# Optimization experiments

Measured on AMD Instinct MI355X. Metric: run time of the kernel, lower is better.

Reference implementation:

```python
import jax, jax.numpy as jnp
import numpy as np

NC = 80
CENTER_RADIUS = 2.5
TOPK = 10
BOX_W, CLS_W, OBJ_W = 7.5, 0.5, 1.0
ALPHA, GAMMA = 0.25, 2.0
EPS = 1e-7
BIG = 1e10


def _corners(b):
    x, y, w, h = b[..., 0], b[..., 1], b[..., 2], b[..., 3]
    return x - w / 2, y - h / 2, x + w / 2, y + h / 2


def _pairwise_iou(b1, b2):
    # b1: (N,4) xywh, b2: (G,4) xywh -> (N,G) plain IoU
    x11, y11, x12, y12 = [t[:, None] for t in _corners(b1)]
    x21, y21, x22, y22 = _corners(b2)
    inter = jnp.clip(jnp.minimum(x12, x22) - jnp.maximum(x11, x21), 0) * \
            jnp.clip(jnp.minimum(y12, y22) - jnp.maximum(y11, y21), 0)
    union = (b1[:, 2] * b1[:, 3])[:, None] + (b2[:, 2] * b2[:, 3])[None, :] - inter + EPS
    return inter / union


def _ciou(b1, b2):
    # aligned boxes (N,4),(N,4) xywh -> (N,) CIoU
    x11, y11, x12, y12 = _corners(b1)
    x21, y21, x22, y22 = _corners(b2)
    w1, h1 = b1[..., 2], b1[..., 3]
    w2, h2 = b2[..., 2], b2[..., 3]
    inter = jnp.clip(jnp.minimum(x12, x22) - jnp.maximum(x11, x21), 0) * \
            jnp.clip(jnp.minimum(y12, y22) - jnp.maximum(y11, y21), 0)
    union = w1 * h1 + w2 * h2 - inter + EPS
    iou = inter / union
    cw = jnp.maximum(x12, x22) - jnp.minimum(x11, x21)
    ch = jnp.maximum(y12, y22) - jnp.minimum(y11, y21)
    c2 = cw ** 2 + ch ** 2 + EPS
    rho2 = ((x11 + x12 - x21 - x22) ** 2 + (y11 + y12 - y21 - y22) ** 2) / 4
    v = (4.0 / jnp.pi ** 2) * (jnp.arctan(w2 / (h2 + EPS)) - jnp.arctan(w1 / (h1 + EPS))) ** 2
    alpha = jax.lax.stop_gradient(v / (v - iou + (1.0 + EPS)))
    return iou - (rho2 / c2 + v * alpha)


def _assign(pred_boxes, pred_scores, gt_boxes, gt_classes, anchor_centers):
    # SimOTA: returns fg mask (N,) bool and matched gt index per anchor (N,)
    N = pred_boxes.shape[0]
    G = gt_boxes.shape[0]
    d = jnp.sqrt(jnp.sum((anchor_centers[:, None, :] - gt_boxes[None, :, :2]) ** 2, -1))
    cand = (d < CENTER_RADIUS).any(axis=1)                      # (N,) center prior
    cand = jnp.where(cand.any(), cand, jnp.ones_like(cand))     # fallback: all anchors
    n_cand = cand.sum().astype(jnp.int32)
    iou = _pairwise_iou(pred_boxes, gt_boxes)                   # (N,G)
    iou = jnp.where(cand[:, None], iou, 0.0)                    # candidates only
    iou_cost = -jnp.log(iou + 1e-8)
    # cls cost: BCE-with-logits of sigmoid scores vs one-hot gt, summed over classes.
    # sum_c bce(s_c, y_c) = sum_c softplus(s_c) - s_{gt}; avoids (N,G,nc) tensor.
    sp_sum = jax.nn.softplus(pred_scores).sum(axis=1)           # (N,)
    cls_cost = sp_sum[:, None] - pred_scores[:, gt_classes]     # (N,G)
    cost = jnp.where(cand[:, None], iou_cost + 3.0 * cls_cost, BIG)
    # dynamic-k: k_j = clip(floor(sum_i iou[i,j]), 1, min(topk, n_cand))
    dyn_k = jnp.maximum(jnp.floor(iou.sum(axis=0)).astype(jnp.int32), 1)
    dyn_k = jnp.minimum(dyn_k, jnp.minimum(TOPK, n_cand))       # (G,)
    _, topk_idx = jax.lax.top_k(-cost.T, TOPK)                  # (G,TOPK) smallest-cost anchors
    keep = jnp.arange(TOPK)[None, :] < dyn_k[:, None]           # (G,TOPK)
    matching = jnp.zeros((G, N), dtype=bool).at[jnp.arange(G)[:, None], topk_idx].set(keep)
    matching = matching.T                                       # (N,G)
    # conflict resolution: anchors matched to >1 gt keep only min-cost gt
    count = matching.sum(axis=1)
    best = jnp.argmin(jnp.where(matching, cost, BIG), axis=1)
    matching = jnp.where((count > 1)[:, None], jax.nn.one_hot(best, G, dtype=bool), matching)
    fg = matching.any(axis=1)
    matched_gt = jnp.argmax(matching, axis=1)
    return fg, matched_gt


def _image_loss(pred, gt_boxes, gt_classes, anchor_centers):
    pb = pred[:, :4]
    pc = pred[:, 4:4 + NC]
    po = pred[:, -1]
    fg, mgt = _assign(pb, jax.nn.sigmoid(pc), gt_boxes, gt_classes, anchor_centers)
    fg_f = fg.astype(pred.dtype)
    # objectness: BCE-with-logits, mean over anchors
    obj = (jax.nn.softplus(po) - po * fg_f).mean()
    # box: CIoU on matched pairs (masked sum)
    tgt_boxes = gt_boxes[mgt]                                   # (N,4)
    box = jnp.sum((1.0 - _ciou(pb, tgt_boxes)) * fg_f)
    # cls: focal BCE on matched anchors
    tgt_cls = jax.nn.one_hot(gt_classes[mgt], NC, dtype=pred.dtype)
    bce = jax.nn.softplus(pc) - pc * tgt_cls
    p = jax.nn.sigmoid(pc)
    p_t = p * tgt_cls + (1 - p) * (1 - tgt_cls)
    cls = jnp.sum((ALPHA * (1 - p_t) ** GAMMA * bce).sum(axis=1) * fg_f)
    return box, cls, obj, fg_f.sum()


def setup_inputs() -> dict:
    B, N, M = 4, 33600, 100
    key = jax.random.key(0)
    ks = jax.random.split(key, 7)
    boxes_xy = jax.random.uniform(ks[0], (B, N, 2)) * 640.0
    boxes_wh = jax.random.uniform(ks[1], (B, N, 2)) * 100.0 + 10.0
    logits = jax.random.normal(ks[2], (B, N, NC + 1))
    pred = jnp.concatenate([boxes_xy, boxes_wh, logits], axis=-1)    # (B,N,85)
    gt_xy = jax.random.uniform(ks[3], (B, M, 2)) * 640.0
    gt_wh = jax.random.uniform(ks[4], (B, M, 2)) * 100.0 + 10.0
    gt_boxes = jnp.concatenate([gt_xy, gt_wh], axis=-1)              # (B,M,4), all valid (sum>0)
    gt_classes = jax.random.randint(ks[5], (B, M), 0, NC, dtype=jnp.int32)
    anchor_centers = jax.random.uniform(ks[6], (N, 2)) * 640.0
    return {"pred": pred, "gt_boxes": gt_boxes, "gt_classes": gt_classes,
            "anchor_centers": anchor_centers}


def reference(pred, gt_boxes, gt_classes, anchor_centers):
    box, cls, obj, npos = jax.vmap(_image_loss, in_axes=(0, 0, 0, None))(
        pred, gt_boxes, gt_classes, anchor_centers)
    n_pos = jnp.maximum(npos.sum(), 1.0)
    total = BOX_W * box.sum() / n_pos + CLS_W * cls.sum() / n_pos + OBJ_W * obj.sum()
    return total
```

## Files before the change

### kernel.cpp

```cpp
#include <hip/hip_runtime.h>
#include <math.h>

#define B_ 4
#define N_ 33600
#define G_ 100
#define NCLS 80
#define STRIDE 85
#define TK 10
#define NBLK 525

__device__ __forceinline__ float sigmoidf_(float x) {
    return 1.0f / (1.0f + expf(-x));
}
__device__ __forceinline__ float softplusf_(float x) {
    return fmaxf(x, 0.0f) + log1pf(expf(-fabsf(x)));
}
__device__ __forceinline__ float waveRedSum(float v) {
    #pragma unroll
    for (int off = 32; off; off >>= 1) v += __shfl_xor(v, off, 64);
    return v;
}

__global__ void k_cand(const float* __restrict__ gtb,
                       const float* __restrict__ anc,
                       unsigned char* __restrict__ mask,
                       unsigned long long* __restrict__ bkey)
{
    __shared__ float gcx[G_], gcy[G_];
    const int b = blockIdx.y;
    const int tid = threadIdx.x;
    if (tid < G_) {
        gcx[tid] = gtb[(b * G_ + tid) * 4 + 0];
        gcy[tid] = gtb[(b * G_ + tid) * 4 + 1];
    }
    __syncthreads();
    const int n = blockIdx.x * blockDim.x + tid;
    if (n >= N_) return;
    bkey[(size_t)b * N_ + n] = 0xFFFFFFFFFFFFFFFFull;
    const float2 a = ((const float2*)anc)[n];
    int c = 0;
    #pragma unroll 10
    for (int g = 0; g < G_; ++g) {
        const float dx = a.x - gcx[g], dy = a.y - gcy[g];
        c |= (dx * dx + dy * dy < 6.25f) ? 1 : 0;
    }
    mask[b * N_ + n] = (unsigned char)c;
}

__global__ void k_compact(const unsigned char* __restrict__ mask,
                          int* __restrict__ cidx,
                          int* __restrict__ counts)
{
    const int b = blockIdx.x;
    const int tid = threadIdx.x;
    const int lane = tid & 63, wid = tid >> 6;
    __shared__ int wsum[4];
    int base = 0;
    const int CH = 4096;
    for (int chunk = 0; chunk * CH < N_; ++chunk) {
        const int i0 = chunk * CH + tid * 16;
        uint4 v = make_uint4(0, 0, 0, 0);
        if (i0 + 16 <= N_) v = *reinterpret_cast<const uint4*>(mask + (size_t)b * N_ + i0);
        const int cnt = __popc(v.x) + __popc(v.y) + __popc(v.z) + __popc(v.w);
        int incl = cnt;
        #pragma unroll
        for (int off = 1; off < 64; off <<= 1) {
            const int t = __shfl_up(incl, off, 64);
            if (lane >= off) incl += t;
        }
        if (lane == 63) wsum[wid] = incl;
        __syncthreads();
        int wbase = 0;
        for (int w = 0; w < wid; ++w) wbase += wsum[w];
        const int ctot = wsum[0] + wsum[1] + wsum[2] + wsum[3];
        int pos = base + wbase + (incl - cnt);
        if (cnt) {
            const unsigned w4[4] = {v.x, v.y, v.z, v.w};
            #pragma unroll
            for (int j = 0; j < 16; ++j) {
                if ((w4[j >> 2] >> ((j & 3) * 8)) & 1u)
                    cidx[(size_t)b * N_ + pos++] = i0 + j;
            }
        }
        base += ctot;
        __syncthreads();
    }
    if (tid == 0) {
        counts[b * 2 + 0] = base;
        counts[b * 2 + 1] = (base == 0) ? 1 : 0;
    }
}

__global__ void k_cfeat(const float* __restrict__ pred,
                        const int* __restrict__ cidx,
                        const int* __restrict__ counts,
                        float* __restrict__ cfeat)
{
    const int b = blockIdx.y;
    const int cnt = counts[b * 2 + 0];
    const int allc = counts[b * 2 + 1];
    if (allc) return;
    const int tid = threadIdx.x;
    const int lane = tid & 63, wid = tid >> 6;
    const int wavesPerImg = gridDim.x * (blockDim.x >> 6);
    const int w0 = blockIdx.x * (blockDim.x >> 6) + wid;
    for (int i = w0; i < cnt; i += wavesPerImg) {
        const int n = cidx[(size_t)b * N_ + i];
        const float* row = pred + (size_t)(b * N_ + n) * STRIDE;
        float s = softplusf_(sigmoidf_(row[4 + lane]));
        if (lane < NCLS - 64) s += softplusf_(sigmoidf_(row[4 + 64 + lane]));
        s = waveRedSum(s);
        if (lane == 0) {
            const float px = row[0], py = row[1], pw = row[2], ph = row[3];
            float* cf = cfeat + (size_t)(b * N_ + i) * 8;
            cf[0] = px - pw * 0.5f;
            cf[1] = py - ph * 0.5f;
            cf[2] = px + pw * 0.5f;
            cf[3] = py + ph * 0.5f;
            cf[4] = pw * ph;
            cf[5] = s;
        }
    }
}

__global__ void __launch_bounds__(64)
k_topk(const float* __restrict__ pred,
       const float* __restrict__ gtb,
       const int* __restrict__ gtc,
       const int* __restrict__ cidx,
       const int* __restrict__ counts,
       const float* __restrict__ cfeat,
       unsigned long long* __restrict__ bkey)
{
    const int b = blockIdx.y, g = blockIdx.x;
    const int lane = threadIdx.x;
    const int cnt = counts[b * 2 + 0];
    const int allc = counts[b * 2 + 1];
    const int count = allc ? N_ : cnt;

    const float* gb = gtb + (b * G_ + g) * 4;
    const float gxc = gb[0], gyc = gb[1], gw = gb[2], gh = gb[3];
    const float gx1 = gxc - gw * 0.5f, gy1 = gyc - gh * 0.5f;
    const float gx2 = gxc + gw * 0.5f, gy2 = gyc + gh * 0.5f;
    const float garea = gw * gh;
    const int cls = gtc[b * G_ + g];

    float kcost[TK];
    int   kslot[TK];
    #pragma unroll
    for (int j = 0; j < TK; ++j) { kcost[j] = INFINITY; kslot[j] = 0x7FFFFFFF; }

    float iousum = 0.0f;
    for (int i = lane; i < count; i += 64) {
        float x1, y1, x2, y2, parea, sp;
        int n;
        if (allc) {
            n = i;
            const float* pr = pred + (size_t)(b * N_ + n) * STRIDE;
            const float px = pr[0], py = pr[1], pw = pr[2], ph = pr[3];
            x1 = px - pw * 0.5f; y1 = py - ph * 0.5f;
            x2 = px + pw * 0.5f; y2 = py + ph * 0.5f;
            parea = pw * ph;
            float s = 0.0f;
            for (int cc = 0; cc < NCLS; ++cc) s += softplusf_(sigmoidf_(pr[4 + cc]));
            sp = s;
        } else {
            n = cidx[(size_t)b * N_ + i];
            const float* cf = cfeat + (size_t)(b * N_ + i) * 8;
            x1 = cf[0]; y1 = cf[1]; x2 = cf[2]; y2 = cf[3];
            parea = cf[4]; sp = cf[5];
        }
        const float iw = fmaxf(fminf(x2, gx2) - fmaxf(x1, gx1), 0.0f);
        const float ih = fmaxf(fminf(y2, gy2) - fmaxf(y1, gy1), 0.0f);
        const float inter = iw * ih;
        const float uni = parea + garea - inter + 1e-7f;
        const float iou = inter / uni;
        iousum += iou;
        const float sgc = sigmoidf_(pred[(size_t)(b * N_ + n) * STRIDE + 4 + cls]);
        float c = -logf(iou + 1e-8f) + 3.0f * (sp - sgc);
        int   s = i;
        #pragma unroll
        for (int j = 0; j < TK; ++j) {
            const bool lt = (c < kcost[j]);
            const float tc = kcost[j]; const int ts = kslot[j];
            if (lt) { kcost[j] = c; kslot[j] = s; c = tc; s = ts; }
        }
    }

    #pragma unroll
    for (int off = 32; off; off >>= 1) iousum += __shfl_xor(iousum, off, 64);

    unsigned long long win[TK];
    #pragma unroll
    for (int r = 0; r < TK; ++r) {
        const unsigned long long mykey =
            ((unsigned long long)__float_as_uint(kcost[0]) << 32) | (unsigned)kslot[0];
        unsigned long long k2 = mykey;
        #pragma unroll
        for (int off = 32; off; off >>= 1) {
            const unsigned long long o = __shfl_xor(k2, off, 64);
            k2 = (o < k2) ? o : k2;
        }
        win[r] = k2;
        if (mykey == k2) {
            #pragma unroll
            for (int j = 0; j < TK - 1; ++j) { kcost[j] = kcost[j + 1]; kslot[j] = kslot[j + 1]; }
            kcost[TK - 1] = INFINITY; kslot[TK - 1] = 0x7FFFFFFF;
        }
    }

    const int kmax = (count < TK) ? count : TK;
    int dk = (int)floorf(iousum);
    if (dk < 1) dk = 1;
    if (dk > kmax) dk = kmax;

    if (lane == 0) {
        #pragma unroll
        for (int r = 0; r < TK; ++r) {
            if (r < dk) {
                const unsigned slot = (unsigned)(win[r] & 0xFFFFFFFFull);
                const int n = allc ? (int)slot : cidx[(size_t)b * N_ + (int)slot];
                const unsigned cbits = (unsigned)(win[r] >> 32);
                const unsigned long long key =
                    ((unsigned long long)cbits << 32) | (unsigned)g;
                atomicMin(&bkey[(size_t)b * N_ + n], key);
            }
        }
    }
}

__global__ void k_objfg(const float* __restrict__ pred,
                        const float* __restrict__ gtb,
                        const int* __restrict__ gtc,
                        const unsigned long long* __restrict__ bkey,
                        float* __restrict__ part)
{
    const int tid = threadIdx.x;
    const unsigned i = blockIdx.x * blockDim.x + tid;
    const int lane = tid & 63, wid = tid >> 6;
    const unsigned long long key = bkey[i];
    const bool fg = (key != 0xFFFFFFFFFFFFFFFFull);
    float so = softplusf_(pred[(size_t)i * STRIDE + (STRIDE - 1)]);
    float posum = 0.0f, box = 0.0f, clsacc = 0.0f, npos = 0.0f;

    unsigned long long m = __ballot(fg);
    while (m) {
        const int src = (int)__ffsll((unsigned long long)m) - 1;
        m &= (m - 1);
        const unsigned ai = (unsigned)__shfl((int)i, src, 64);
        const int mg = __shfl((int)(unsigned)(key & 0xFFFFFFFFull), src, 64);
        const int b = (int)(ai / (unsigned)N_);
        const float* pr = pred + (size_t)ai * STRIDE;
        const int cg = gtc[b * G_ + mg];
        {
            const float x = pr[4 + lane];
            const float t = (lane == cg) ? 1.0f : 0.0f;
            const float bce = softplusf_(x) - x * t;
            const float p = sigmoidf_(x);
            const float pt = t * p + (1.0f - t) * (1.0f - p);
            const float om = 1.0f - pt;
            clsacc += 0.25f * om * om * bce;
        }
        if (lane < NCLS - 64) {
            const float x = pr[4 + 64 + lane];
            const float t = ((64 + lane) == cg) ? 1.0f : 0.0f;
            const float bce = softplusf_(x) - x * t;
            const float p = sigmoidf_(x);
            const float pt = t * p + (1.0f - t) * (1.0f - p);
            const float om = 1.0f - pt;
            clsacc += 0.25f * om * om * bce;
        }
        if (lane == 0) {
            npos += 1.0f;
            posum += pr[STRIDE - 1];
            const float* gb = gtb + (b * G_ + mg) * 4;
            const float px = pr[0], py = pr[1], pw = pr[2], ph = pr[3];
            const float gx = gb[0], gy = gb[1], gw = gb[2], gh = gb[3];
            const float x11 = px - pw * 0.5f, y11 = py - ph * 0.5f;
            const float x12 = px + pw * 0.5f, y12 = py + ph * 0.5f;
            const float x21 = gx - gw * 0.5f, y21 = gy - gh * 0.5f;
            const float x22 = gx + gw * 0.5f, y22 = gy + gh * 0.5f;
            const float iw = fmaxf(fminf(x12, x22) - fmaxf(x11, x21), 0.0f);
            const float ih = fmaxf(fminf(y12, y22) - fmaxf(y11, y21), 0.0f);
            const float inter = iw * ih;
            const float uni = pw * ph + gw * gh - inter + 1e-7f;
            const float iou = inter / uni;
            const float cw = fmaxf(x12, x22) - fminf(x11, x21);
            const float chh = fmaxf(y12, y22) - fminf(y11, y21);
            const float c2 = cw * cw + chh * chh + 1e-7f;
            const float ddx = x11 + x12 - x21 - x22;
            const float ddy = y11 + y12 - y21 - y22;
            const float rho2 = (ddx * ddx + ddy * ddy) * 0.25f;
            const float dv = atanf(gw / (gh + 1e-7f)) - atanf(pw / (ph + 1e-7f));
            const float v = (float)(4.0 / (M_PI * M_PI)) * dv * dv;
            const float alpha = v / (v - iou + 1.0f + 1e-7f);
            const float ciou = iou - (rho2 / c2 + v * alpha);
            box += 1.0f - ciou;
        }
    }

    so = waveRedSum(so);
    posum = waveRedSum(posum);
    box = waveRedSum(box);
    clsacc = waveRedSum(clsacc);
    npos = waveRedSum(npos);
    __shared__ float ws[4][5];
    if (lane == 0) {
        ws[wid][0] = so; ws[wid][1] = posum; ws[wid][2] = box;
        ws[wid][3] = clsacc; ws[wid][4] = npos;
    }
    __syncthreads();
    if (tid == 0) {
        float r[5];
        #pragma unroll
        for (int k = 0; k < 5; ++k)
            r[k] = ws[0][k] + ws[1][k] + ws[2][k] + ws[3][k];
        float4* p = (float4*)part;
        p[blockIdx.x * 2 + 0] = make_float4(r[0], r[1], r[2], r[3]);
        p[blockIdx.x * 2 + 1] = make_float4(r[4], 0.0f, 0.0f, 0.0f);
    }
}

__global__ void k_final(const float* __restrict__ part, int nblocks,
                        float* __restrict__ out)
{
    const int tid = threadIdx.x;
    float so = 0, sp = 0, sb = 0, sc = 0, sn = 0;
    for (int i = tid; i < nblocks; i += 256) {
        const float4 a = ((const float4*)part)[i * 2 + 0];
        const float4 b = ((const float4*)part)[i * 2 + 1];
        so += a.x; sp += a.y; sb += a.z; sc += a.w; sn += b.x;
    }
    __shared__ float red[256];
    float in5[5] = {so, sp, sb, sc, sn};
    float res[5];
    #pragma unroll
    for (int k = 0; k < 5; ++k) {
        red[tid] = in5[k];
        __syncthreads();
        for (int s = 128; s > 0; s >>= 1) {
            if (tid < s) red[tid] += red[tid + s];
            __syncthreads();
        }
        res[k] = red[0];
        __syncthreads();
    }
    if (tid == 0) {
        const float obj_sum = res[0] - res[1];
        const float n_pos = fmaxf(res[4], 1.0f);
        const float total = 7.5f * res[2] / n_pos
                          + 0.5f * res[3] / n_pos
                          + obj_sum / (float)N_;
        out[0] = total;
    }
}

extern "C" void kernel_launch(void* const* d_in, const int* in_sizes, int n_in,
                              void* d_out, int out_size, void* d_ws, size_t ws_size,
                              hipStream_t stream)
{
    const float* pred = (const float*)d_in[0];
    const float* gtb  = (const float*)d_in[1];
    const int*   gtc  = (const int*)d_in[2];
    const float* anc  = (const float*)d_in[3];

    char* ws = (char*)d_ws;
    size_t off = 0;
    auto take = [&](size_t bytes) {
        size_t o = off;
        off += (bytes + 255) & ~(size_t)255;
        return o;
    };
    unsigned char*      mask   = (unsigned char*)(ws + take((size_t)B_ * N_));
    int*                cidx   = (int*)(ws + take((size_t)B_ * N_ * 4));
    int*                counts = (int*)(ws + take((size_t)B_ * 2 * 4));
    unsigned long long* bkey   = (unsigned long long*)(ws + take((size_t)B_ * N_ * 8));
    float*              cfeat  = (float*)(ws + take((size_t)B_ * N_ * 8 * 4));
    float*              part   = (float*)(ws + take((size_t)NBLK * 8 * 4));

    const int nblkA = (N_ + 255) / 256;
    dim3 gA(nblkA, B_);
    k_cand<<<gA, 256, 0, stream>>>(gtb, anc, mask, bkey);
    k_compact<<<B_, 256, 0, stream>>>(mask, cidx, counts);
    dim3 gS(32, B_);
    k_cfeat<<<gS, 256, 0, stream>>>(pred, cidx, counts, cfeat);
    dim3 gT(G_, B_);
    k_topk<<<gT, 64, 0, stream>>>(pred, gtb, gtc, cidx, counts, cfeat, bkey);
    k_objfg<<<NBLK, 256, 0, stream>>>(pred, gtb, gtc, bkey, part);
    k_final<<<1, 256, 0, stream>>>(part, NBLK, (float*)d_out);
}
```

Before: 44.13 us.

## Fuse candidate softplus sums and objectness into prep kernel, last-block final reduction

Measured after the change: 51.56 us. +16.9%, slower.

```diff
diff --git a/kernel.cpp b/kernel.cpp
--- a/kernel.cpp
+++ b/kernel.cpp
@@ -7,7 +7,8 @@
 #define NCLS 80
 #define STRIDE 85
 #define TK 10
-#define NBLK 525
+#define K1BLK 132
+#define K4BLK 525
 
 __device__ __forceinline__ float sigmoidf_(float x) {
     return 1.0f / (1.0f + expf(-x));
@@ -21,35 +22,62 @@
     return v;
 }
 
-__global__ void k_cand(const float* __restrict__ gtb,
-                       const float* __restrict__ anc,
-                       unsigned char* __restrict__ mask,
-                       unsigned long long* __restrict__ bkey)
+__global__ void k1_prep(const float* __restrict__ gtb,
+                        const float* __restrict__ anc,
+                        const float* __restrict__ pred,
+                        unsigned char* __restrict__ mask,
+                        float* __restrict__ spsum,
+                        unsigned long long* __restrict__ bkey,
+                        float* __restrict__ pobj,
+                        unsigned int* __restrict__ done)
 {
     __shared__ float gcx[G_], gcy[G_];
     const int b = blockIdx.y;
     const int tid = threadIdx.x;
+    const int lane = tid & 63, wid = tid >> 6;
+    if (blockIdx.x == 0 && b == 0 && tid == 0) *done = 0u;
     if (tid < G_) {
         gcx[tid] = gtb[(b * G_ + tid) * 4 + 0];
         gcy[tid] = gtb[(b * G_ + tid) * 4 + 1];
     }
     __syncthreads();
     const int n = blockIdx.x * blockDim.x + tid;
-    if (n >= N_) return;
-    bkey[(size_t)b * N_ + n] = 0xFFFFFFFFFFFFFFFFull;
-    const float2 a = ((const float2*)anc)[n];
-    int c = 0;
-    #pragma unroll 10
-    for (int g = 0; g < G_; ++g) {
-        const float dx = a.x - gcx[g], dy = a.y - gcy[g];
-        c |= (dx * dx + dy * dy < 6.25f) ? 1 : 0;
-    }
-    mask[b * N_ + n] = (unsigned char)c;
-}
-
-__global__ void k_compact(const unsigned char* __restrict__ mask,
-                          int* __restrict__ cidx,
-                          int* __restrict__ counts)
+    float so = 0.0f;
+    if (n < N_) {
+        const size_t a_ = (size_t)b * N_ + n;
+        bkey[a_] = 0xFFFFFFFFFFFFFFFFull;
+        so = softplusf_(pred[a_ * STRIDE + (STRIDE - 1)]);
+        const float2 a = ((const float2*)anc)[n];
+        int c = 0;
+        #pragma unroll 10
+        for (int g = 0; g < G_; ++g) {
+            const float dx = a.x - gcx[g], dy = a.y - gcy[g];
+            c |= (dx * dx + dy * dy < 6.25f) ? 1 : 0;
+        }
+        mask[a_] = (unsigned char)c;
+        unsigned long long m = __ballot(c != 0);
+        while (m) {
+            const int src = (int)__ffsll(m) - 1;
+            m &= (m - 1);
+            const int an = __shfl(n, src, 64);
+            const float* row = pred + ((size_t)b * N_ + an) * STRIDE + 4;
+            float s = softplusf_(sigmoidf_(row[lane]));
+            if (lane < NCLS - 64) s += softplusf_(sigmoidf_(row[64 + lane]));
+            s = waveRedSum(s);
+            if (lane == 0) spsum[(size_t)b * N_ + an] = s;
+        }
+    }
+    so = waveRedSum(so);
+    __shared__ float ws[4];
+    if (lane == 0) ws[wid] = so;
+    __syncthreads();
+    if (tid == 0)
+        pobj[b * K1BLK + blockIdx.x] = ws[0] + ws[1] + ws[2] + ws[3];
+}
+
+__global__ void k2_compact(const unsigned char* __restrict__ mask,
+                           int* __restrict__ cidx,
+                           int* __restrict__ counts)
 {
     const int b = blockIdx.x;
     const int tid = threadIdx.x;
@@ -91,46 +119,14 @@
     }
 }
 
-__global__ void k_cfeat(const float* __restrict__ pred,
-                        const int* __restrict__ cidx,
-                        const int* __restrict__ counts,
-                        float* __restrict__ cfeat)
-{
-    const int b = blockIdx.y;
-    const int cnt = counts[b * 2 + 0];
-    const int allc = counts[b * 2 + 1];
-    if (allc) return;
-    const int tid = threadIdx.x;
-    const int lane = tid & 63, wid = tid >> 6;
-    const int wavesPerImg = gridDim.x * (blockDim.x >> 6);
-    const int w0 = blockIdx.x * (blockDim.x >> 6) + wid;
-    for (int i = w0; i < cnt; i += wavesPerImg) {
-        const int n = cidx[(size_t)b * N_ + i];
-        const float* row = pred + (size_t)(b * N_ + n) * STRIDE;
-        float s = softplusf_(sigmoidf_(row[4 + lane]));
-        if (lane < NCLS - 64) s += softplusf_(sigmoidf_(row[4 + 64 + lane]));
-        s = waveRedSum(s);
-        if (lane == 0) {
-            const float px = row[0], py = row[1], pw = row[2], ph = row[3];
-            float* cf = cfeat + (size_t)(b * N_ + i) * 8;
-            cf[0] = px - pw * 0.5f;
-            cf[1] = py - ph * 0.5f;
-            cf[2] = px + pw * 0.5f;
-            cf[3] = py + ph * 0.5f;
-            cf[4] = pw * ph;
-            cf[5] = s;
-        }
-    }
-}
-
 __global__ void __launch_bounds__(64)
-k_topk(const float* __restrict__ pred,
-       const float* __restrict__ gtb,
-       const int* __restrict__ gtc,
-       const int* __restrict__ cidx,
-       const int* __restrict__ counts,
-       const float* __restrict__ cfeat,
-       unsigned long long* __restrict__ bkey)
+k3_topk(const float* __restrict__ pred,
+        const float* __restrict__ gtb,
+        const int* __restrict__ gtc,
+        const int* __restrict__ cidx,
+        const int* __restrict__ counts,
+        const float* __restrict__ spsum,
+        unsigned long long* __restrict__ bkey)
 {
     const int b = blockIdx.y, g = blockIdx.x;
     const int lane = threadIdx.x;
@@ -152,31 +148,26 @@
 
     float iousum = 0.0f;
     for (int i = lane; i < count; i += 64) {
-        float x1, y1, x2, y2, parea, sp;
-        int n;
+        const int n = allc ? i : cidx[(size_t)b * N_ + i];
+        const float* pr = pred + (size_t)(b * N_ + n) * STRIDE;
+        const float px = pr[0], py = pr[1], pw = pr[2], ph = pr[3];
+        const float x1 = px - pw * 0.5f, y1 = py - ph * 0.5f;
+        const float x2 = px + pw * 0.5f, y2 = py + ph * 0.5f;
+        float sp;
         if (allc) {
-            n = i;
-            const float* pr = pred + (size_t)(b * N_ + n) * STRIDE;
-            const float px = pr[0], py = pr[1], pw = pr[2], ph = pr[3];
-            x1 = px - pw * 0.5f; y1 = py - ph * 0.5f;
-            x2 = px + pw * 0.5f; y2 = py + ph * 0.5f;
-            parea = pw * ph;
             float s = 0.0f;
             for (int cc = 0; cc < NCLS; ++cc) s += softplusf_(sigmoidf_(pr[4 + cc]));
             sp = s;
         } else {
-            n = cidx[(size_t)b * N_ + i];
-            const float* cf = cfeat + (size_t)(b * N_ + i) * 8;
-            x1 = cf[0]; y1 = cf[1]; x2 = cf[2]; y2 = cf[3];
-            parea = cf[4]; sp = cf[5];
+            sp = spsum[(size_t)b * N_ + n];
         }
         const float iw = fmaxf(fminf(x2, gx2) - fmaxf(x1, gx1), 0.0f);
         const float ih = fmaxf(fminf(y2, gy2) - fmaxf(y1, gy1), 0.0f);
         const float inter = iw * ih;
-        const float uni = parea + garea - inter + 1e-7f;
+        const float uni = pw * ph + garea - inter + 1e-7f;
         const float iou = inter / uni;
         iousum += iou;
-        const float sgc = sigmoidf_(pred[(size_t)(b * N_ + n) * STRIDE + 4 + cls]);
+        const float sgc = sigmoidf_(pr[4 + cls]);
         float c = -logf(iou + 1e-8f) + 3.0f * (sp - sgc);
         int   s = i;
         #pragma unroll
@@ -229,32 +220,34 @@
     }
 }
 
-__global__ void k_objfg(const float* __restrict__ pred,
-                        const float* __restrict__ gtb,
-                        const int* __restrict__ gtc,
-                        const unsigned long long* __restrict__ bkey,
-                        float* __restrict__ part)
+__global__ void k4_fg(const float* __restrict__ pred,
+                      const float* __restrict__ gtb,
+                      const int* __restrict__ gtc,
+                      const unsigned long long* __restrict__ bkey,
+                      const float* __restrict__ pobj,
+                      float* __restrict__ pfg,
+                      unsigned int* __restrict__ done,
+                      float* __restrict__ out)
 {
     const int tid = threadIdx.x;
     const unsigned i = blockIdx.x * blockDim.x + tid;
     const int lane = tid & 63, wid = tid >> 6;
     const unsigned long long key = bkey[i];
     const bool fg = (key != 0xFFFFFFFFFFFFFFFFull);
-    float so = softplusf_(pred[(size_t)i * STRIDE + (STRIDE - 1)]);
     float posum = 0.0f, box = 0.0f, clsacc = 0.0f, npos = 0.0f;
 
     unsigned long long m = __ballot(fg);
     while (m) {
-        const int src = (int)__ffsll((unsigned long long)m) - 1;
+        const int src = (int)__ffsll(m) - 1;
         m &= (m - 1);
         const unsigned ai = (unsigned)__shfl((int)i, src, 64);
         const int mg = __shfl((int)(unsigned)(key & 0xFFFFFFFFull), src, 64);
         const int b = (int)(ai / (unsigned)N_);
         const float* pr = pred + (size_t)ai * STRIDE;
-        const int cg = gtc[b * G_ + mg];
+        const int cg_ = gtc[b * G_ + mg];
         {
             const float x = pr[4 + lane];
-            const float t = (lane == cg) ? 1.0f : 0.0f;
+            const float t = (lane == cg_) ? 1.0f : 0.0f;
             const float bce = softplusf_(x) - x * t;
             const float p = sigmoidf_(x);
             const float pt = t * p + (1.0f - t) * (1.0f - p);
@@ -263,7 +256,7 @@
         }
         if (lane < NCLS - 64) {
             const float x = pr[4 + 64 + lane];
-            const float t = ((64 + lane) == cg) ? 1.0f : 0.0f;
+            const float t = ((64 + lane) == cg_) ? 1.0f : 0.0f;
             const float bce = softplusf_(x) - x * t;
             const float p = sigmoidf_(x);
             const float pt = t * p + (1.0f - t) * (1.0f - p);
@@ -299,37 +292,39 @@
         }
     }
 
-    so = waveRedSum(so);
     posum = waveRedSum(posum);
     box = waveRedSum(box);
     clsacc = waveRedSum(clsacc);
     npos = waveRedSum(npos);
-    __shared__ float ws[4][5];
+    __shared__ float ws[4][4];
     if (lane == 0) {
-        ws[wid][0] = so; ws[wid][1] = posum; ws[wid][2] = box;
-        ws[wid][3] = clsacc; ws[wid][4] = npos;
+        ws[wid][0] = posum; ws[wid][1] = box;
+        ws[wid][2] = clsacc; ws[wid][3] = npos;
     }
     __syncthreads();
+    __shared__ int amlast;
     if (tid == 0) {
-        float r[5];
-        #pragma unroll
-        for (int k = 0; k < 5; ++k)
-            r[k] = ws[0][k] + ws[1][k] + ws[2][k] + ws[3][k];
-        float4* p = (float4*)part;
-        p[blockIdx.x * 2 + 0] = make_float4(r[0], r[1], r[2], r[3]);
-        p[blockIdx.x * 2 + 1] = make_float4(r[4], 0.0f, 0.0f, 0.0f);
-    }
-}
-
-__global__ void k_final(const float* __restrict__ part, int nblocks,
-                        float* __restrict__ out)
-{
-    const int tid = threadIdx.x;
+        float* p = pfg + (size_t)blockIdx.x * 4;
+        #pragma unroll
+        for (int k = 0; k < 4; ++k) {
+            const float v = ws[0][k] + ws[1][k] + ws[2][k] + ws[3][k];
+            __hip_atomic_store(&p[k], v, __ATOMIC_RELAXED, __HIP_MEMORY_SCOPE_AGENT);
+        }
+        const unsigned prev = __hip_atomic_fetch_add(done, 1u, __ATOMIC_ACQ_REL,
+                                                     __HIP_MEMORY_SCOPE_AGENT);
+        amlast = (prev == (unsigned)(K4BLK - 1)) ? 1 : 0;
+    }
+    __syncthreads();
+    if (!amlast) return;
+
     float so = 0, sp = 0, sb = 0, sc = 0, sn = 0;
-    for (int i = tid; i < nblocks; i += 256) {
-        const float4 a = ((const float4*)part)[i * 2 + 0];
-        const float4 b = ((const float4*)part)[i * 2 + 1];
-        so += a.x; sp += a.y; sb += a.z; sc += a.w; sn += b.x;
+    for (int k = tid; k < B_ * K1BLK; k += 256) so += pobj[k];
+    for (int k = tid; k < K4BLK; k += 256) {
+        const float* p = pfg + (size_t)k * 4;
+        sp += __hip_atomic_load(&p[0], __ATOMIC_RELAXED, __HIP_MEMORY_SCOPE_AGENT);
+        sb += __hip_atomic_load(&p[1], __ATOMIC_RELAXED, __HIP_MEMORY_SCOPE_AGENT);
+        sc += __hip_atomic_load(&p[2], __ATOMIC_RELAXED, __HIP_MEMORY_SCOPE_AGENT);
+        sn += __hip_atomic_load(&p[3], __ATOMIC_RELAXED, __HIP_MEMORY_SCOPE_AGENT);
     }
     __shared__ float red[256];
     float in5[5] = {so, sp, sb, sc, sn};
@@ -348,10 +343,9 @@
     if (tid == 0) {
         const float obj_sum = res[0] - res[1];
         const float n_pos = fmaxf(res[4], 1.0f);
-        const float total = 7.5f * res[2] / n_pos
-                          + 0.5f * res[3] / n_pos
-                          + obj_sum / (float)N_;
-        out[0] = total;
+        out[0] = 7.5f * res[2] / n_pos
+               + 0.5f * res[3] / n_pos
+               + obj_sum / (float)N_;
     }
 }
 
@@ -375,17 +369,16 @@
     int*                cidx   = (int*)(ws + take((size_t)B_ * N_ * 4));
     int*                counts = (int*)(ws + take((size_t)B_ * 2 * 4));
     unsigned long long* bkey   = (unsigned long long*)(ws + take((size_t)B_ * N_ * 8));
-    float*              cfeat  = (float*)(ws + take((size_t)B_ * N_ * 8 * 4));
-    float*              part   = (float*)(ws + take((size_t)NBLK * 8 * 4));
-
-    const int nblkA = (N_ + 255) / 256;
-    dim3 gA(nblkA, B_);
-    k_cand<<<gA, 256, 0, stream>>>(gtb, anc, mask, bkey);
-    k_compact<<<B_, 256, 0, stream>>>(mask, cidx, counts);
-    dim3 gS(32, B_);
-    k_cfeat<<<gS, 256, 0, stream>>>(pred, cidx, counts, cfeat);
-    dim3 gT(G_, B_);
-    k_topk<<<gT, 64, 0, stream>>>(pred, gtb, gtc, cidx, counts, cfeat, bkey);
-    k_objfg<<<NBLK, 256, 0, stream>>>(pred, gtb, gtc, bkey, part);
-    k_final<<<1, 256, 0, stream>>>(part, NBLK, (float*)d_out);
-}
+    float*              spsum  = (float*)(ws + take((size_t)B_ * N_ * 4));
+    float*              pobj   = (float*)(ws + take((size_t)B_ * K1BLK * 4));
+    float*              pfg    = (float*)(ws + take((size_t)K4BLK * 4 * 4));
+    unsigned int*       done   = (unsigned int*)(ws + take(4));
+
+    dim3 g1(K1BLK, B_);
+    k1_prep<<<g1, 256, 0, stream>>>(gtb, anc, pred, mask, spsum, bkey, pobj, done);
+    k2_compact<<<B_, 256, 0, stream>>>(mask, cidx, counts);
+    dim3 g3(G_, B_);
+    k3_topk<<<g3, 64, 0, stream>>>(pred, gtb, gtc, cidx, counts, spsum, bkey);
+    k4_fg<<<K4BLK, 256, 0, stream>>>(pred, gtb, gtc, bkey, pobj, pfg, done,
+                                     (float*)d_out);
+}
```
